# Kernel tuning notes

Measured on AMD Instinct MI355X. Metric: run time of the kernel, lower is better.

The kernel has to match this reference:

```python
import jax, jax.numpy as jnp
import numpy as np

TOP_K = 30
NUM_RBF = 16
MAX_REL = 32  # max_relative_feature
LN_EPS = 1e-5


def normalize(x, axis=-1, eps=1e-12):
    n = jnp.linalg.norm(x, axis=axis, keepdims=True)
    return x / jnp.maximum(n, eps)


def gather_nodes(nodes, idx):
    # nodes [B,L,C], idx [B,L,K] -> [B,L,K,C]
    B, L, K = idx.shape
    flat = idx.reshape(B, L * K)
    g = jnp.take_along_axis(nodes, flat[:, :, None], axis=1)
    return g.reshape(B, L, K, -1)


def gather_edges(edges, idx):
    # edges [B,L,L,C], idx [B,L,K] -> [B,L,K,C]
    return jnp.take_along_axis(edges, idx[..., None], axis=2)


def _dist(Xca, mask, eps=1e-6):
    mask_2D = mask[:, None, :] * mask[:, :, None]            # [B,L,L]
    dX = Xca[:, None, :, :] - Xca[:, :, None, :]             # [B,L,L,3]
    D = mask_2D * jnp.sqrt(jnp.sum(dX ** 2, -1) + eps)
    D_max = jnp.max(D, -1, keepdims=True)
    D_adjust = D + (1.0 - mask_2D) * D_max
    k = min(TOP_K, Xca.shape[1])
    neg_vals, E_idx = jax.lax.top_k(-D_adjust, k)            # smallest-k
    D_neighbors = -neg_vals
    mask_neighbors = gather_edges(mask_2D[..., None], E_idx)
    return D_neighbors, E_idx, mask_neighbors


def _rbf(D):
    D_mu = jnp.linspace(2.0, 22.0, NUM_RBF)                  # [R]
    D_sigma = (22.0 - 2.0) / NUM_RBF
    return jnp.exp(-(((D[..., None] - D_mu) / D_sigma) ** 2))


def _quaternions(R):
    # R [...,3,3] -> Q [...,4]
    diag = jnp.diagonal(R, axis1=-2, axis2=-1)               # [...,3]
    Rxx, Ryy, Rzz = diag[..., 0], diag[..., 1], diag[..., 2]
    mags = 0.5 * jnp.sqrt(jnp.abs(1 + jnp.stack(
        [Rxx - Ryy - Rzz, -Rxx + Ryy - Rzz, -Rxx - Ryy + Rzz], -1)))
    signs = jnp.sign(jnp.stack([
        R[..., 2, 1] - R[..., 1, 2],
        R[..., 0, 2] - R[..., 2, 0],
        R[..., 1, 0] - R[..., 0, 1]], -1))
    xyz = signs * mags
    w = jnp.sqrt(jax.nn.relu(1 + jnp.sum(diag, -1, keepdims=True))) / 2.0
    return normalize(jnp.concatenate([xyz, w], -1))


def _get_orientations(A, B, C, E_idx, eps=1e-6):
    v1 = A - B
    v2 = C - B
    e1 = v1 / (jnp.linalg.norm(v1, axis=-1, keepdims=True) + eps)
    u2 = v2 - jnp.sum(e1 * v2, -1, keepdims=True) * e1
    e2 = u2 / (jnp.linalg.norm(u2, axis=-1, keepdims=True) + eps)
    e3 = jnp.cross(e1, e2)
    O = jnp.stack([e1, e2, e3], axis=-1)                     # [B,L,3,3] columns
    O9 = O.reshape(O.shape[0], O.shape[1], 9)
    O_nb = gather_nodes(O9, E_idx).reshape(*E_idx.shape, 3, 3)  # [B,L,K,3,3]
    B_nb = gather_nodes(B, E_idx)                            # [B,L,K,3]
    dX = B_nb - B[:, :, None, :]
    dU = normalize(jnp.einsum('blij,blkj->blki', O, dX))
    R = jnp.einsum('blji,blkjm->blkim', O, O_nb)             # O^T @ O_nb
    Q = _quaternions(R)
    return jnp.concatenate([dU, Q], -1)                      # [B,L,K,7]


def _AD_features(Xca, eps=1e-6):
    dX = Xca[:, 1:, :] - Xca[:, :-1, :]
    U = normalize(dX)
    u_2, u_1, u_0 = U[:, :-2], U[:, 1:-1], U[:, 2:]
    n_2 = normalize(jnp.cross(u_2, u_1))
    n_1 = normalize(jnp.cross(u_1, u_0))
    cosA = jnp.clip(-jnp.sum(u_1 * u_0, -1), -1 + eps, 1 - eps)
    A = jnp.arccos(cosA)
    cosD = jnp.clip(jnp.sum(n_2 * n_1, -1), -1 + eps, 1 - eps)
    D = jnp.sign(jnp.sum(u_2 * n_1, -1)) * jnp.arccos(cosD)
    AD = jnp.stack([jnp.cos(A), jnp.sin(A) * jnp.cos(D), jnp.sin(A) * jnp.sin(D)], 2)
    return jnp.pad(AD, ((0, 0), (1, 2), (0, 0)))             # [B,L,3]


def layer_norm(x, g, b):
    mu = jnp.mean(x, -1, keepdims=True)
    var = jnp.var(x, -1, keepdims=True)
    return (x - mu) / jnp.sqrt(var + LN_EPS) * g + b


def setup_inputs() -> dict:
    key = jax.random.key(0)
    ks = jax.random.split(key, 12)
    B, L = 4, 2048
    node_f, edge_f = 128, 128
    edge_in = 16 + NUM_RBF + 7 + 16  # 55 ('coarse')
    s = lambda fan: 1.0 / np.sqrt(fan)
    return {
        'X': jax.random.normal(ks[0], (B, L, 4, 3), jnp.float32),
        'mask': jnp.ones((B, L), jnp.float32),
        'residue_idx': jnp.arange(B * L, dtype=jnp.int32).reshape(B, L),
        'chain_labels': jax.random.randint(ks[1], (B, L), 0, 2, jnp.int32),
        'W_pe': jax.random.uniform(ks[2], (2 * MAX_REL + 1, 16), jnp.float32, -s(65), s(65)),
        'b_pe': jnp.zeros((16,), jnp.float32),
        'W_ch': jax.random.uniform(ks[3], (2, 16), jnp.float32, -s(2), s(2)),
        'b_ch': jnp.zeros((16,), jnp.float32),
        'W_node': jax.random.uniform(ks[4], (3, node_f), jnp.float32, -s(3), s(3)),
        'b_node': jnp.zeros((node_f,), jnp.float32),
        'W_edge': jax.random.uniform(ks[5], (edge_in, edge_f), jnp.float32, -s(edge_in), s(edge_in)),
        'b_edge': jnp.zeros((edge_f,), jnp.float32),
        'g_nodes': jnp.ones((node_f,), jnp.float32),
        'bn_nodes': jnp.zeros((node_f,), jnp.float32),
        'g_edges': jnp.ones((edge_f,), jnp.float32),
        'bn_edges': jnp.zeros((edge_f,), jnp.float32),
    }


def reference(X, mask, residue_idx, chain_labels, W_pe, b_pe, W_ch, b_ch,
              W_node, b_node, W_edge, b_edge, g_nodes, bn_nodes, g_edges, bn_edges):
    N, Ca, C = X[:, :, 0], X[:, :, 1], X[:, :, 2]
    D_neighbors, E_idx, mask_neighbors = _dist(Ca, mask)
    RBF = _rbf(D_neighbors)                                  # [B,L,K,16]
    O_features = _get_orientations(N, Ca, C, E_idx)          # [B,L,K,7]
    # positional encodings from residue-index offsets
    res_nb = jnp.take_along_axis(residue_idx[:, :, None].repeat(E_idx.shape[2], 2) * 0 +
                                 gather_nodes(residue_idx[..., None], E_idx)[..., 0], E_idx * 0, axis=2)
    res_nb = gather_nodes(residue_idx[..., None], E_idx)[..., 0]
    offset = res_nb - residue_idx[:, :, None]
    d = jnp.clip(offset + MAX_REL, 0, 2 * MAX_REL)
    E_positional = W_pe[d] + b_pe                            # [B,L,K,16]
    # chain embedding from same/other-chain indicator
    ch_nb = gather_nodes(chain_labels[..., None], E_idx)[..., 0]
    same = (ch_nb == chain_labels[:, :, None]).astype(jnp.float32)
    E_chains = jnp.stack([same, 1.0 - same], -1) @ W_ch + b_ch  # [B,L,K,16]
    E = jnp.concatenate([E_positional, RBF, O_features, E_chains], -1)
    E = layer_norm(E @ W_edge + b_edge, g_edges, bn_edges)
    V = _AD_features(Ca)                                     # [B,L,3]
    V = layer_norm(V @ W_node + b_node, g_nodes, bn_nodes)
    return V, E, E_idx
```

## Files before the change

kernel.cpp:

```cpp
#include <hip/hip_runtime.h>

#define NB 4
#define NL 2048
#define NK 30
#define NRES (NB*NL)
#define NEDGE (NRES*NK)
#define EPB 64

enum : int {
  WOFF_DNB   = 0,
  WOFF_EIDX  = 245760,
  WOFF_O     = 491520,
  WOFF_WPE   = 565248,
  WOFF_BPE   = 566288,
  WOFF_WCH   = 566304,
  WOFF_BCH   = 566336,
  WOFF_WNODE = 566352,
  WOFF_BNODE = 566736,
  WOFF_WEDGE = 566864,
  WOFF_BEDGE = 573904,
  WOFF_GN    = 574032,
  WOFF_BNN   = 574160,
  WOFF_GE    = 574288,
  WOFF_BNE   = 574416,
  WOFF_PK    = 574544,
};

__device__ __forceinline__ float sgnf(float x) {
  return (x > 0.f) ? 1.f : ((x < 0.f) ? -1.f : 0.f);
}
__device__ __forceinline__ float loadf(const void* p, int idx, bool isbf) {
  if (isbf) return __uint_as_float(((unsigned)((const unsigned short*)p)[idx]) << 16);
  return ((const float*)p)[idx];
}
__device__ __forceinline__ int geti(const void* p, int idx, int mode) {
  if (mode == 0) return ((const int*)p)[idx];
  if (mode == 1) return (int)rintf(((const float*)p)[idx]);
  return (int)rintf(__uint_as_float(((unsigned)((const unsigned short*)p)[idx]) << 16));
}
__device__ __forceinline__ bool probe_bf(const void* maskp) {
  return ((const unsigned*)maskp)[0] == 0x3F803F80u;
}
__device__ __forceinline__ int probe_int(const void* residxp) {
  unsigned w1 = ((const unsigned*)residxp)[1];
  return (w1 == 1u) ? 0 : ((w1 == 0x3F800000u) ? 1 : 2);
}
__device__ __forceinline__ unsigned long long shfl_xor_u64(unsigned long long x, int m) {
  int lo = (int)(unsigned)(x & 0xffffffffull);
  int hi = (int)(unsigned)(x >> 32);
  lo = __shfl_xor(lo, m, 64);
  hi = __shfl_xor(hi, m, 64);
  return ((unsigned long long)(unsigned)hi << 32) | (unsigned)lo;
}

struct ConvArgs {
  const void* src[12];
  int off[12];
  int sz[12];
  const void* maskp;
};

__global__ void pf_kernel(ConvArgs a, const void* Xraw, float* wsf) {
  const bool isbf = probe_bf(a.maskp);
  const int t = threadIdx.x;
  if (blockIdx.x < 32) {
    const int r = blockIdx.x * 256 + t;
    const int xb = r * 12;
    float nx = loadf(Xraw, xb+0, isbf), ny = loadf(Xraw, xb+1, isbf), nz = loadf(Xraw, xb+2, isbf);
    float cax= loadf(Xraw, xb+3, isbf), cay= loadf(Xraw, xb+4, isbf), caz= loadf(Xraw, xb+5, isbf);
    float cx = loadf(Xraw, xb+6, isbf), cy = loadf(Xraw, xb+7, isbf), cz = loadf(Xraw, xb+8, isbf);
    float mk = loadf(a.maskp, r, isbf);
    float4* pko = (float4*)(wsf + WOFF_PK);
    pko[r] = make_float4(cax, cay, caz, mk);
    float v1x=nx-cax, v1y=ny-cay, v1z=nz-caz;
    float v2x=cx-cax, v2y=cy-cay, v2z=cz-caz;
    float n1 = sqrtf(v1x*v1x + v1y*v1y + v1z*v1z) + 1e-6f;
    float e1x=v1x/n1, e1y=v1y/n1, e1z=v1z/n1;
    float dp = e1x*v2x + e1y*v2y + e1z*v2z;
    float u2x=v2x-dp*e1x, u2y=v2y-dp*e1y, u2z=v2z-dp*e1z;
    float n2 = sqrtf(u2x*u2x + u2y*u2y + u2z*u2z) + 1e-6f;
    float e2x=u2x/n2, e2y=u2y/n2, e2z=u2z/n2;
    float e3x = e1y*e2z - e1z*e2y;
    float e3y = e1z*e2x - e1x*e2z;
    float e3z = e1x*e2y - e1y*e2x;
    float* o = wsf + WOFF_O + (size_t)r*9;
    o[0]=e1x; o[1]=e2x; o[2]=e3x;
    o[3]=e1y; o[4]=e2y; o[5]=e3y;
    o[6]=e1z; o[7]=e2z; o[8]=e3z;
  } else {
    const int stride = 40 * 256;
    const int t0 = (blockIdx.x - 32) * 256 + t;
    for (int q = 0; q < 12; ++q) {
      float* dst = wsf + a.off[q];
      const int n = a.sz[q];
      for (int i = t0; i < n; i += stride) dst[i] = loadf(a.src[q], i, isbf);
    }
  }
}

#define CE(i,j) { unsigned long long a_=q[i], b_=q[j]; bool lt_=a_<b_; \
                  q[i]=lt_?a_:b_; q[j]=lt_?b_:a_; }
#define SORT8(B) CE(B+0,B+1) CE(B+2,B+3) CE(B+4,B+5) CE(B+6,B+7) \
                 CE(B+0,B+2) CE(B+1,B+3) CE(B+4,B+6) CE(B+5,B+7) \
                 CE(B+1,B+2) CE(B+5,B+6) \
                 CE(B+0,B+4) CE(B+1,B+5) CE(B+2,B+6) CE(B+3,B+7) \
                 CE(B+2,B+4) CE(B+3,B+5) \
                 CE(B+1,B+2) CE(B+3,B+4) CE(B+5,B+6)
#define SHIFTQ(B) { q[B+0]=q[B+1]; q[B+1]=q[B+2]; q[B+2]=q[B+3]; q[B+3]=q[B+4]; \
                    q[B+4]=q[B+5]; q[B+5]=q[B+6]; q[B+6]=q[B+7]; q[B+7]=~0ull; }

__device__ __forceinline__ void topk_body(int blk, const float* wsf, int* eidx, float* dnb,
                                          float* outf, unsigned long long outEidx) {
#pragma clang fp contract(off)
  const int lane = threadIdx.x & 63;
  const int row = blk*4 + (threadIdx.x >> 6);
  const int b = row >> 11, i = row & (NL-1);
  const float4* pb = ((const float4*)(wsf + WOFF_PK)) + b*NL;
  const float4 pi = pb[i];
  const float xi = pi.x, yi = pi.y, zi = pi.z, mi = pi.w;
  unsigned long long q[32];
  float lmax = -1e30f;
  #pragma unroll
  for (int s=0;s<32;s++){
    float4 pj = pb[s*64 + lane];
    float dx=pj.x-xi, dy=pj.y-yi, dz=pj.z-zi;
    float ss = dx*dx;
    ss = ss + dy*dy;
    ss = ss + dz*dz;
    ss = ss + 1e-6f;
    float m2 = mi*pj.w;
    float d = m2 * sqrtf(ss);
    lmax = fmaxf(lmax, d);
    q[s] = ((unsigned long long)__float_as_uint(d) << 32) | (unsigned)(s*64 + lane);
  }
  #pragma unroll
  for (int m=1;m<64;m<<=1) lmax = fmaxf(lmax, __shfl_xor(lmax, m, 64));
  const unsigned dmb = __float_as_uint(lmax);
  #pragma unroll
  for (int s=0;s<32;s++)
    if ((unsigned)(q[s] >> 32) == 0u)
      q[s] = ((unsigned long long)dmb << 32) | (unsigned)q[s];
  SORT8(0) SORT8(8) SORT8(16) SORT8(24)
  const size_t obase = (size_t)row*NK;
  #pragma unroll 1
  for (int k=0;k<NK;k++){
    unsigned long long c01 = q[0]  < q[8]  ? q[0]  : q[8];
    unsigned long long c23 = q[16] < q[24] ? q[16] : q[24];
    unsigned long long cand = c01 < c23 ? c01 : c23;
    float dh = __uint_as_float((unsigned)(cand >> 32));
    float dmin = dh;
    #pragma unroll
    for (int m=1;m<64;m<<=1) dmin = fminf(dmin, __shfl_xor(dmin, m, 64));
    unsigned long long bal = __ballot(dh == dmin);
    unsigned long long best;
    if (__popcll(bal) == 1) {
      int src = __ffsll((long long)bal) - 1;
      int lo = __shfl((int)(unsigned)cand, src, 64);
      best = ((unsigned long long)__float_as_uint(dmin) << 32) | (unsigned)lo;
    } else {
      best = cand;
      #pragma unroll
      for (int m=1;m<64;m<<=1){
        unsigned long long o2 = shfl_xor_u64(best, m);
        best = o2 < best ? o2 : best;
      }
    }
    if (lane==0){
      unsigned j = (unsigned)best;
      eidx[obase + k] = (int)j;
      dnb[obase + k] = __uint_as_float((unsigned)(best >> 32));
      outf[outEidx + obase + k] = (float)j;
    }
    if (cand == best){
      if      (q[0]  == best) SHIFTQ(0)
      else if (q[8]  == best) SHIFTQ(8)
      else if (q[16] == best) SHIFTQ(16)
      else                    SHIFTQ(24)
    }
  }
}

__device__ __forceinline__ void node_body(int blk, const float* wsf, const void* Xraw,
                                          const void* maskp, float* outf) {
  const bool isbf = probe_bf(maskp);
  const int gw = (blk * 256 + (int)threadIdx.x) >> 6;
  const int lane = threadIdx.x & 63;
  const int b = gw / NL, l = gw % NL;
  float ad0 = 0.f, ad1 = 0.f, ad2 = 0.f;
  if (l >= 1 && l <= NL - 3) {
    const int base = (b*NL)*12;
    float p0x = loadf(Xraw, base+(l-1)*12+3, isbf), p0y = loadf(Xraw, base+(l-1)*12+4, isbf), p0z = loadf(Xraw, base+(l-1)*12+5, isbf);
    float p1x = loadf(Xraw, base+(l  )*12+3, isbf), p1y = loadf(Xraw, base+(l  )*12+4, isbf), p1z = loadf(Xraw, base+(l  )*12+5, isbf);
    float p2x = loadf(Xraw, base+(l+1)*12+3, isbf), p2y = loadf(Xraw, base+(l+1)*12+4, isbf), p2z = loadf(Xraw, base+(l+1)*12+5, isbf);
    float p3x = loadf(Xraw, base+(l+2)*12+3, isbf), p3y = loadf(Xraw, base+(l+2)*12+4, isbf), p3z = loadf(Xraw, base+(l+2)*12+5, isbf);
    float u2x=p1x-p0x, u2y=p1y-p0y, u2z=p1z-p0z;
    float u1x=p2x-p1x, u1y=p2y-p1y, u1z=p2z-p1z;
    float u0x=p3x-p2x, u0y=p3y-p2y, u0z=p3z-p2z;
    float nn;
    nn = fmaxf(sqrtf(u2x*u2x+u2y*u2y+u2z*u2z), 1e-12f); u2x/=nn; u2y/=nn; u2z/=nn;
    nn = fmaxf(sqrtf(u1x*u1x+u1y*u1y+u1z*u1z), 1e-12f); u1x/=nn; u1y/=nn; u1z/=nn;
    nn = fmaxf(sqrtf(u0x*u0x+u0y*u0y+u0z*u0z), 1e-12f); u0x/=nn; u0y/=nn; u0z/=nn;
    float n2x = u2y*u1z - u2z*u1y, n2y = u2z*u1x - u2x*u1z, n2z = u2x*u1y - u2y*u1x;
    float n1x = u1y*u0z - u1z*u0y, n1y = u1z*u0x - u1x*u0z, n1z = u1x*u0y - u1y*u0x;
    nn = fmaxf(sqrtf(n2x*n2x+n2y*n2y+n2z*n2z), 1e-12f); n2x/=nn; n2y/=nn; n2z/=nn;
    nn = fmaxf(sqrtf(n1x*n1x+n1y*n1y+n1z*n1z), 1e-12f); n1x/=nn; n1y/=nn; n1z/=nn;
    const float lo = (float)(-1.0 + 1e-6), hi = (float)(1.0 - 1e-6);
    float cosA = -(u1x*u0x + u1y*u0y + u1z*u0z);
    cosA = fminf(fmaxf(cosA, lo), hi);
    float A = acosf(cosA);
    float cosD = n2x*n1x + n2y*n1y + n2z*n1z;
    cosD = fminf(fmaxf(cosD, lo), hi);
    float Dd = sgnf(u2x*n1x + u2y*n1y + u2z*n1z) * acosf(cosD);
    ad0 = cosf(A);
    ad1 = sinf(A) * cosf(Dd);
    ad2 = sinf(A) * sinf(Dd);
  }
  const int c0 = 2*lane, c1 = c0 + 1;
  float acc0 = wsf[WOFF_BNODE+c0] + ad0*wsf[WOFF_WNODE+c0] + ad1*wsf[WOFF_WNODE+128+c0] + ad2*wsf[WOFF_WNODE+256+c0];
  float acc1 = wsf[WOFF_BNODE+c1] + ad0*wsf[WOFF_WNODE+c1] + ad1*wsf[WOFF_WNODE+128+c1] + ad2*wsf[WOFF_WNODE+256+c1];
  float s = acc0 + acc1;
  for (int m=1;m<64;m<<=1) s += __shfl_xor(s, m, 64);
  float mu_ = s * (1.0f/128.0f);
  float d0 = acc0 - mu_, d1 = acc1 - mu_;
  float v = d0*d0 + d1*d1;
  for (int m=1;m<64;m<<=1) v += __shfl_xor(v, m, 64);
  float inv = 1.0f / sqrtf(v * (1.0f/128.0f) + 1e-5f);
  float y0 = d0*inv*wsf[WOFF_GN + c0] + wsf[WOFF_BNN + c0];
  float y1 = d1*inv*wsf[WOFF_GN + c1] + wsf[WOFF_BNN + c1];
  float2 pk; pk.x = y0; pk.y = y1;
  *((float2*)(outf + (size_t)gw*128 + c0)) = pk;
}

__global__ __launch_bounds__(256, 4) void tn_kernel(const float* wsf, int* eidx, float* dnb,
                                                 float* outf, unsigned long long outEidx,
                                                 const void* Xraw, const void* maskp) {
  if (blockIdx.x < NRES/4) topk_body(blockIdx.x, wsf, eidx, dnb, outf, outEidx);
  else                     node_body(blockIdx.x - NRES/4, wsf, Xraw, maskp, outf);
}

__global__ __launch_bounds__(256) void edge_kernel(const float* wsf, const int* eidx,
                                                   const void* Xraw, const void* maskp,
                                                   const void* residx, const void* chains,
                                                   float* outf, unsigned long long outE) {
  __shared__ float F[55][EPB];
  const bool isbf = probe_bf(maskp);
  const int icmode = probe_int(residx);
  const int t = threadIdx.x;
  const int g = t & 63, sq = t >> 6;
  const int e = blockIdx.x * EPB + g;
  const int row = e / NK;
  const int b = row / NL, i = row % NL;
  const int j = eidx[e];
  const int ri = geti(residx, b*NL + i, icmode), rj = geti(residx, b*NL + j, icmode);
  int dd = rj - ri + 32;
  dd = dd < 0 ? 0 : (dd > 64 ? 64 : dd);
  const int ci = geti(chains, b*NL + i, icmode), cj = geti(chains, b*NL + j, icmode);
  const float D = wsf[WOFF_DNB + e];
  #pragma unroll
  for (int u = 0; u < 4; ++u) {
    const int s = sq*4 + u;
    F[s][g] = wsf[WOFF_WPE + dd*16 + s] + wsf[WOFF_BPE + s];
    float mu = (float)(2.0 + s * (20.0 / 15.0));
    float tt = (D - mu) / 1.25f;
    F[16+s][g] = expf(-(tt*tt));
    float w = (ci == cj) ? wsf[WOFF_WCH + s] : wsf[WOFF_WCH + 16 + s];
    F[39+s][g] = w + wsf[WOFF_BCH + s];
  }
  if (g < 16) {
    const int gq = sq*16 + g;
    const int eq = blockIdx.x * EPB + gq;
    const int rowq = eq / NK;
    const int bq = rowq / NL;
    const int jq = eidx[eq];
    const float* Oi = wsf + WOFF_O + (size_t)rowq*9;
    const float* Oj = wsf + WOFF_O + ((size_t)(bq*NL + jq))*9;
    const int ci_ = rowq*12 + 3, cj_ = (bq*NL + jq)*12 + 3;
    float dx = loadf(Xraw, cj_+0, isbf) - loadf(Xraw, ci_+0, isbf);
    float dy = loadf(Xraw, cj_+1, isbf) - loadf(Xraw, ci_+1, isbf);
    float dz = loadf(Xraw, cj_+2, isbf) - loadf(Xraw, ci_+2, isbf);
    float du0 = Oi[0]*dx + Oi[1]*dy + Oi[2]*dz;
    float du1 = Oi[3]*dx + Oi[4]*dy + Oi[5]*dz;
    float du2 = Oi[6]*dx + Oi[7]*dy + Oi[8]*dz;
    float n = fmaxf(sqrtf(du0*du0 + du1*du1 + du2*du2), 1e-12f);
    F[32][gq] = du0/n; F[33][gq] = du1/n; F[34][gq] = du2/n;
    float R[3][3];
    #pragma unroll
    for (int a2=0;a2<3;a2++)
      #pragma unroll
      for (int m=0;m<3;m++)
        R[a2][m] = Oi[0*3+a2]*Oj[0*3+m] + Oi[1*3+a2]*Oj[1*3+m] + Oi[2*3+a2]*Oj[2*3+m];
    float mx = 0.5f*sqrtf(fabsf(1.0f + R[0][0] - R[1][1] - R[2][2]));
    float my = 0.5f*sqrtf(fabsf(1.0f - R[0][0] + R[1][1] - R[2][2]));
    float mz = 0.5f*sqrtf(fabsf(1.0f - R[0][0] - R[1][1] + R[2][2]));
    float qx = sgnf(R[2][1]-R[1][2]) * mx;
    float qy = sgnf(R[0][2]-R[2][0]) * my;
    float qz = sgnf(R[1][0]-R[0][1]) * mz;
    float qw = sqrtf(fmaxf(1.0f + R[0][0] + R[1][1] + R[2][2], 0.0f)) / 2.0f;
    float qn = fmaxf(sqrtf(qx*qx + qy*qy + qz*qz + qw*qw), 1e-12f);
    F[35][gq] = qx/qn; F[36][gq] = qy/qn; F[37][gq] = qz/qn; F[38][gq] = qw/qn;
  }
  __syncthreads();
  const int wv = t >> 6, lane = t & 63;
  const int eg = lane >> 4;
  const int cg = lane & 15;
  const int ebase = wv*16 + eg*4;
  const int c0 = cg*8;
  const float4* W4 = (const float4*)(wsf + WOFF_WEDGE);
  const float4 beA = *(const float4*)(wsf + WOFF_BEDGE + c0);
  const float4 beB = *(const float4*)(wsf + WOFF_BEDGE + c0 + 4);
  float acc[4][8];
  #pragma unroll
  for (int qq=0;qq<4;qq++){
    acc[qq][0]=beA.x; acc[qq][1]=beA.y; acc[qq][2]=beA.z; acc[qq][3]=beA.w;
    acc[qq][4]=beB.x; acc[qq][5]=beB.y; acc[qq][6]=beB.z; acc[qq][7]=beB.w;
  }
  for (int d = 0; d < 55; ++d) {
    float4 f  = *(const float4*)&F[d][ebase];
    float4 wa = W4[d*32 + cg*2];
    float4 wb = W4[d*32 + cg*2 + 1];
    #pragma unroll
    for (int qq=0;qq<4;qq++){
      float fq = (qq==0)?f.x:(qq==1)?f.y:(qq==2)?f.z:f.w;
      acc[qq][0] = fmaf(fq, wa.x, acc[qq][0]);
      acc[qq][1] = fmaf(fq, wa.y, acc[qq][1]);
      acc[qq][2] = fmaf(fq, wa.z, acc[qq][2]);
      acc[qq][3] = fmaf(fq, wa.w, acc[qq][3]);
      acc[qq][4] = fmaf(fq, wb.x, acc[qq][4]);
      acc[qq][5] = fmaf(fq, wb.y, acc[qq][5]);
      acc[qq][6] = fmaf(fq, wb.z, acc[qq][6]);
      acc[qq][7] = fmaf(fq, wb.w, acc[qq][7]);
    }
  }
  const float4 geA = *(const float4*)(wsf + WOFF_GE + c0);
  const float4 geB = *(const float4*)(wsf + WOFF_GE + c0 + 4);
  const float4 bnA = *(const float4*)(wsf + WOFF_BNE + c0);
  const float4 bnB = *(const float4*)(wsf + WOFF_BNE + c0 + 4);
  #pragma unroll
  for (int qq=0;qq<4;qq++){
    float s = ((acc[qq][0]+acc[qq][1])+(acc[qq][2]+acc[qq][3]))
            + ((acc[qq][4]+acc[qq][5])+(acc[qq][6]+acc[qq][7]));
    s += __shfl_xor(s, 1, 64); s += __shfl_xor(s, 2, 64);
    s += __shfl_xor(s, 4, 64); s += __shfl_xor(s, 8, 64);
    float mu_ = s * (1.0f/128.0f);
    float dv[8];
    #pragma unroll
    for (int jj=0;jj<8;jj++) dv[jj] = acc[qq][jj] - mu_;
    float v = ((dv[0]*dv[0]+dv[1]*dv[1])+(dv[2]*dv[2]+dv[3]*dv[3]))
            + ((dv[4]*dv[4]+dv[5]*dv[5])+(dv[6]*dv[6]+dv[7]*dv[7]));
    v += __shfl_xor(v, 1, 64); v += __shfl_xor(v, 2, 64);
    v += __shfl_xor(v, 4, 64); v += __shfl_xor(v, 8, 64);
    float inv = 1.0f / sqrtf(v * (1.0f/128.0f) + 1e-5f);
    float4 oA, oB;
    oA.x = dv[0]*inv*geA.x + bnA.x; oA.y = dv[1]*inv*geA.y + bnA.y;
    oA.z = dv[2]*inv*geA.z + bnA.z; oA.w = dv[3]*inv*geA.w + bnA.w;
    oB.x = dv[4]*inv*geB.x + bnB.x; oB.y = dv[5]*inv*geB.y + bnB.y;
    oB.z = dv[6]*inv*geB.z + bnB.z; oB.w = dv[7]*inv*geB.w + bnB.w;
    float* op = outf + outE + (size_t)(blockIdx.x*EPB + ebase + qq)*128 + c0;
    *(float4*)op       = oA;
    *(float4*)(op + 4) = oB;
  }
}

extern "C" void kernel_launch(void* const* d_in, const int* in_sizes, int n_in,
                              void* d_out, int out_size, void* d_ws, size_t ws_size,
                              hipStream_t stream) {
  float* wsf = (float*)d_ws;
  int* eidx = (int*)(wsf + WOFF_EIDX);
  float* dnb = wsf + WOFF_DNB;
  float* outf = (float*)d_out;
  const void* Xraw = d_in[0];
  const void* maskp = d_in[1];

  unsigned long long outEidx = (unsigned long long)out_size - NEDGE;
  unsigned long long outE    = outEidx - (unsigned long long)NEDGE*128;

  ConvArgs ca;
  const int fsz[12]  = {1040, 16, 32, 16, 384, 128, 7040, 128, 128, 128, 128, 128};
  const int foff[12] = {WOFF_WPE, WOFF_BPE, WOFF_WCH, WOFF_BCH, WOFF_WNODE, WOFF_BNODE,
                        WOFF_WEDGE, WOFF_BEDGE, WOFF_GN, WOFF_BNN, WOFF_GE, WOFF_BNE};
  for (int q = 0; q < 12; ++q) { ca.src[q] = d_in[4 + q]; ca.off[q] = foff[q]; ca.sz[q] = fsz[q]; }
  ca.maskp = maskp;

  pf_kernel<<<72, 256, 0, stream>>>(ca, Xraw, wsf);
  tn_kernel<<<NRES/4 + NRES/4, 256, 0, stream>>>(wsf, eidx, dnb, outf, outEidx, Xraw, maskp);
  edge_kernel<<<NEDGE/EPB, 256, 0, stream>>>(wsf, eidx, Xraw, maskp, d_in[2], d_in[3], outf, outE);
}
```

Before: 292.9 us.

## Precompute positional and chain embedding projections as lookup tables for edge GEMM

The positional (65 offsets) and chain (2 values) embeddings are linear in one-hot inputs, so their product with W_edge, plus the bias, is folded into small tables in the prep kernel. The edge kernel then starts each accumulator from a table lookup indexed by clipped offset and same-chain flag. Its shared-memory feature matrix shrinks from 55 to 23 rows, which cuts the per-edge FMA loop and shared-memory traffic. The cost is extra prep blocks and a changed floating-point summation order.

```diff
diff --git a/kernel.cpp b/kernel.cpp
--- a/kernel.cpp
+++ b/kernel.cpp
@@ -6,6 +6,7 @@
 #define NRES (NB*NL)
 #define NEDGE (NRES*NK)
 #define EPB 64
+#define KD 23
 
 enum : int {
   WOFF_DNB   = 0,
@@ -24,6 +25,8 @@
   WOFF_GE    = 574288,
   WOFF_BNE   = 574416,
   WOFF_PK    = 574544,
+  WOFF_P2    = 607312,
+  WOFF_C2    = 615632,
 };
 
 __device__ __forceinline__ float sgnf(float x) {
@@ -87,13 +90,33 @@
     o[0]=e1x; o[1]=e2x; o[2]=e3x;
     o[3]=e1y; o[4]=e2y; o[5]=e3y;
     o[6]=e1z; o[7]=e2z; o[8]=e3z;
-  } else {
+  } else if (blockIdx.x < 72) {
     const int stride = 40 * 256;
     const int t0 = (blockIdx.x - 32) * 256 + t;
     for (int q = 0; q < 12; ++q) {
       float* dst = wsf + a.off[q];
       const int n = a.sz[q];
       for (int i = t0; i < n; i += stride) dst[i] = loadf(a.src[q], i, isbf);
+    }
+  } else {
+    const int o = (blockIdx.x - 72) * 256 + t;
+    if (o < 65*128) {
+      const int dd = o >> 7, c = o & 127;
+      float sum = loadf(a.src[7], c, isbf);
+      #pragma unroll
+      for (int s = 0; s < 16; ++s)
+        sum += (loadf(a.src[0], dd*16 + s, isbf) + loadf(a.src[1], s, isbf))
+               * loadf(a.src[6], s*128 + c, isbf);
+      wsf[WOFF_P2 + o] = sum;
+    } else if (o < 65*128 + 256) {
+      const int idx = o - 65*128;
+      const int k = idx >> 7, c = idx & 127;
+      float sum = 0.f;
+      #pragma unroll
+      for (int s = 0; s < 16; ++s)
+        sum += (loadf(a.src[2], k*16 + s, isbf) + loadf(a.src[3], s, isbf))
+               * loadf(a.src[6], (39+s)*128 + c, isbf);
+      wsf[WOFF_C2 + idx] = sum;
     }
   }
 }
@@ -242,7 +265,9 @@
                                                    const void* Xraw, const void* maskp,
                                                    const void* residx, const void* chains,
                                                    float* outf, unsigned long long outE) {
-  __shared__ float F[55][EPB];
+  __shared__ float F[KD][EPB];
+  __shared__ int   ddL[EPB];
+  __shared__ int   skL[EPB];
   const bool isbf = probe_bf(maskp);
   const int icmode = probe_int(residx);
   const int t = threadIdx.x;
@@ -250,21 +275,22 @@
   const int e = blockIdx.x * EPB + g;
   const int row = e / NK;
   const int b = row / NL, i = row % NL;
-  const int j = eidx[e];
-  const int ri = geti(residx, b*NL + i, icmode), rj = geti(residx, b*NL + j, icmode);
-  int dd = rj - ri + 32;
-  dd = dd < 0 ? 0 : (dd > 64 ? 64 : dd);
-  const int ci = geti(chains, b*NL + i, icmode), cj = geti(chains, b*NL + j, icmode);
   const float D = wsf[WOFF_DNB + e];
+  if (sq == 0) {
+    const int j = eidx[e];
+    const int ri = geti(residx, b*NL + i, icmode), rj = geti(residx, b*NL + j, icmode);
+    int dd = rj - ri + 32;
+    dd = dd < 0 ? 0 : (dd > 64 ? 64 : dd);
+    const int ci = geti(chains, b*NL + i, icmode), cj = geti(chains, b*NL + j, icmode);
+    ddL[g] = dd;
+    skL[g] = (ci == cj) ? 0 : 1;
+  }
   #pragma unroll
   for (int u = 0; u < 4; ++u) {
     const int s = sq*4 + u;
-    F[s][g] = wsf[WOFF_WPE + dd*16 + s] + wsf[WOFF_BPE + s];
     float mu = (float)(2.0 + s * (20.0 / 15.0));
     float tt = (D - mu) / 1.25f;
-    F[16+s][g] = expf(-(tt*tt));
-    float w = (ci == cj) ? wsf[WOFF_WCH + s] : wsf[WOFF_WCH + 16 + s];
-    F[39+s][g] = w + wsf[WOFF_BCH + s];
+    F[s][g] = expf(-(tt*tt));
   }
   if (g < 16) {
     const int gq = sq*16 + g;
@@ -282,7 +308,7 @@
     float du1 = Oi[3]*dx + Oi[4]*dy + Oi[5]*dz;
     float du2 = Oi[6]*dx + Oi[7]*dy + Oi[8]*dz;
     float n = fmaxf(sqrtf(du0*du0 + du1*du1 + du2*du2), 1e-12f);
-    F[32][gq] = du0/n; F[33][gq] = du1/n; F[34][gq] = du2/n;
+    F[16][gq] = du0/n; F[17][gq] = du1/n; F[18][gq] = du2/n;
     float R[3][3];
     #pragma unroll
     for (int a2=0;a2<3;a2++)
@@ -297,7 +323,7 @@
     float qz = sgnf(R[1][0]-R[0][1]) * mz;
     float qw = sqrtf(fmaxf(1.0f + R[0][0] + R[1][1] + R[2][2], 0.0f)) / 2.0f;
     float qn = fmaxf(sqrtf(qx*qx + qy*qy + qz*qz + qw*qw), 1e-12f);
-    F[35][gq] = qx/qn; F[36][gq] = qy/qn; F[37][gq] = qz/qn; F[38][gq] = qw/qn;
+    F[19][gq] = qx/qn; F[20][gq] = qy/qn; F[21][gq] = qz/qn; F[22][gq] = qw/qn;
   }
   __syncthreads();
   const int wv = t >> 6, lane = t & 63;
@@ -306,18 +332,21 @@
   const int ebase = wv*16 + eg*4;
   const int c0 = cg*8;
   const float4* W4 = (const float4*)(wsf + WOFF_WEDGE);
-  const float4 beA = *(const float4*)(wsf + WOFF_BEDGE + c0);
-  const float4 beB = *(const float4*)(wsf + WOFF_BEDGE + c0 + 4);
   float acc[4][8];
   #pragma unroll
   for (int qq=0;qq<4;qq++){
-    acc[qq][0]=beA.x; acc[qq][1]=beA.y; acc[qq][2]=beA.z; acc[qq][3]=beA.w;
-    acc[qq][4]=beB.x; acc[qq][5]=beB.y; acc[qq][6]=beB.z; acc[qq][7]=beB.w;
-  }
-  for (int d = 0; d < 55; ++d) {
+    const int ed = ebase + qq;
+    const float* p2 = wsf + WOFF_P2 + ddL[ed]*128 + c0;
+    const float* c2 = wsf + WOFF_C2 + skL[ed]*128 + c0;
+    float4 pA = *(const float4*)p2, pB = *(const float4*)(p2+4);
+    float4 cA = *(const float4*)c2, cB = *(const float4*)(c2+4);
+    acc[qq][0]=pA.x+cA.x; acc[qq][1]=pA.y+cA.y; acc[qq][2]=pA.z+cA.z; acc[qq][3]=pA.w+cA.w;
+    acc[qq][4]=pB.x+cB.x; acc[qq][5]=pB.y+cB.y; acc[qq][6]=pB.z+cB.z; acc[qq][7]=pB.w+cB.w;
+  }
+  for (int d = 0; d < KD; ++d) {
     float4 f  = *(const float4*)&F[d][ebase];
-    float4 wa = W4[d*32 + cg*2];
-    float4 wb = W4[d*32 + cg*2 + 1];
+    float4 wa = W4[(16+d)*32 + cg*2];
+    float4 wb = W4[(16+d)*32 + cg*2 + 1];
     #pragma unroll
     for (int qq=0;qq<4;qq++){
       float fq = (qq==0)?f.x:(qq==1)?f.y:(qq==2)?f.z:f.w;
@@ -381,7 +410,7 @@
   for (int q = 0; q < 12; ++q) { ca.src[q] = d_in[4 + q]; ca.off[q] = foff[q]; ca.sz[q] = fsz[q]; }
   ca.maskp = maskp;
 
-  pf_kernel<<<72, 256, 0, stream>>>(ca, Xraw, wsf);
+  pf_kernel<<<106, 256, 0, stream>>>(ca, Xraw, wsf);
   tn_kernel<<<NRES/4 + NRES/4, 256, 0, stream>>>(wsf, eidx, dnb, outf, outEidx, Xraw, maskp);
   edge_kernel<<<NEDGE/EPB, 256, 0, stream>>>(wsf, eidx, Xraw, maskp, d_in[2], d_in[3], outf, outE);
 }
```

After: 271.1 us. 1.08x faster.
